# Kernel optimization log

Measured on AMD Instinct MI355X. Metric: run time of the kernel, lower is better.

## Reference

```python
import jax, jax.numpy as jnp
import numpy as np

K = 27        # 3^3 kernel offsets for kernel_size=3, dimension=3
M = 50000     # kernel-map pairs per offset
N = 100000    # active voxels
C = 64        # channels
EPS = 1e-5


def setup_inputs() -> dict:
    key = jax.random.key(0)
    ks = jax.random.split(key, 5)
    scale = 1.0 / np.sqrt(K * C)
    return {
        "features": jax.random.normal(ks[0], (N, C), jnp.float32),
        "W1": jax.random.normal(ks[1], (K, C, C), jnp.float32) * scale,
        "gamma1": jnp.ones((C,), jnp.float32),
        "beta1": jnp.zeros((C,), jnp.float32),
        "W2": jax.random.normal(ks[2], (K, C, C), jnp.float32) * scale,
        "gamma2": jnp.ones((C,), jnp.float32),
        "beta2": jnp.zeros((C,), jnp.float32),
        "in_maps": jax.random.randint(ks[3], (K, M), 0, N, dtype=jnp.int32),
        "out_maps": jax.random.randint(ks[4], (K, M), 0, N, dtype=jnp.int32),
        "n": N,
    }


def sparse_conv(f, W, in_maps, out_maps, n):
    # gather-GEMM-scatter, the MinkowskiConvolution compute pattern
    gathered = f[in_maps]                              # [K, M, Cin]
    msgs = jnp.einsum('kmc,kcd->kmd', gathered, W)     # [K, M, Cout]
    cout = W.shape[-1]
    out = jnp.zeros((n, cout), f.dtype)
    return out.at[out_maps.reshape(-1)].add(msgs.reshape(-1, cout))


def batch_norm(x, gamma, beta):
    # BatchNorm1d over the [N, C] sparse feature matrix (training-mode batch stats)
    mu = x.mean(axis=0)
    var = x.var(axis=0)
    return (x - mu) * jax.lax.rsqrt(var + EPS) * gamma + beta


def reference(features, W1, gamma1, beta1, W2, gamma2, beta2, in_maps, out_maps, n):
    out = sparse_conv(features, W1, in_maps, out_maps, n)
    out = jax.nn.relu(batch_norm(out, gamma1, beta1))
    out = sparse_conv(out, W2, in_maps, out_maps, n)
    out = batch_norm(out, gamma2, beta2)
    # stride=1 and in_channels==out_channels -> downsample is None
    return jax.nn.relu(out + features)
```

## Files before the change

### kernel.cpp

```cpp
#include <hip/hip_runtime.h>

typedef __attribute__((ext_vector_type(8))) short bf16x8;
typedef __attribute__((ext_vector_type(4))) float f32x4;

#define KK 27
#define MM 50000
#define NV 100000
#define CC 64
#define EPSV 1e-5f
#define PPB 400

__device__ inline void split2(float x, unsigned short& h, unsigned short& l) {
    const unsigned u  = __float_as_uint(x);
    const unsigned hb = u & 0xFFFF0000u;
    h = (unsigned short)(hb >> 16);
    const float r = x - __uint_as_float(hb);
    const unsigned v = __float_as_uint(r);
    l = (unsigned short)((v + 0x7FFFu + ((v >> 16) & 1u)) >> 16);
}

__device__ inline unsigned short rne_bf16(float x) {
    const unsigned u = __float_as_uint(x);
    return (unsigned short)((u + 0x7FFFu + ((u >> 16) & 1u)) >> 16);
}

__global__ __launch_bounds__(256)
void split_planes(const float* __restrict__ x, unsigned short* __restrict__ P) {
    const int i = blockIdx.x * 256 + threadIdx.x;
    const int r = i >> 5, c2 = (i & 31) * 2;
    const float2 v = *(const float2*)(x + (size_t)r * CC + c2);
    unsigned short h0, l0, h1, l1;
    split2(v.x, h0, l0);
    split2(v.y, h1, l1);
    *(unsigned int*)(P + (size_t)r * 128 + c2)      = (unsigned)h0 | ((unsigned)h1 << 16);
    *(unsigned int*)(P + (size_t)r * 128 + 64 + c2) = (unsigned)l0 | ((unsigned)l1 << 16);
}

__global__ __launch_bounds__(256)
void csr_hist(const int* __restrict__ outm, int* __restrict__ cnt) {
    const int e = blockIdx.x * 256 + threadIdx.x;
    if (e < KK * MM) atomicAdd(&cnt[outm[e]], 1);
}

__global__ __launch_bounds__(1024)
void scan1(const int* __restrict__ cnt, int* __restrict__ off, int* __restrict__ bsum) {
    __shared__ int tmp[1024];
    const int t = threadIdx.x;
    const int i = blockIdx.x * 1024 + t;
    const int v = (i < NV) ? cnt[i] : 0;
    tmp[t] = v;
    __syncthreads();
    for (int d = 1; d < 1024; d <<= 1) {
        const int add = (t >= d) ? tmp[t - d] : 0;
        __syncthreads();
        tmp[t] += add;
        __syncthreads();
    }
    if (i < NV) off[i] = tmp[t] - v;
    if (t == 1023) bsum[blockIdx.x] = tmp[1023];
}

__global__ __launch_bounds__(128)
void scan2(int* __restrict__ bsum, int nb) {
    __shared__ int tmp[128];
    const int t = threadIdx.x;
    const int v = (t < nb) ? bsum[t] : 0;
    tmp[t] = v;
    __syncthreads();
    for (int d = 1; d < 128; d <<= 1) {
        const int add = (t >= d) ? tmp[t - d] : 0;
        __syncthreads();
        tmp[t] += add;
        __syncthreads();
    }
    if (t < nb) bsum[t] = tmp[t] - v;
}

__global__ __launch_bounds__(256)
void scan3(int* __restrict__ off, const int* __restrict__ bsum) {
    const int i = blockIdx.x * 256 + threadIdx.x;
    if (i < NV) off[i] += bsum[i >> 10];
    if (i == 0) off[NV] = KK * MM;
}

__global__ __launch_bounds__(256)
void csr_fill(const int* __restrict__ outm, const int* __restrict__ off,
              int* __restrict__ cur, int* __restrict__ dst) {
    const int e = blockIdx.x * 256 + threadIdx.x;
    if (e >= KK * MM) return;
    const int row = outm[e];
    const int pos = atomicAdd(&cur[row], 1);
    dst[e] = off[row] + pos;
}

#define MF(a, b, c) c = __builtin_amdgcn_mfma_f32_16x16x32_bf16(a, b, c, 0, 0, 0)

struct AFrag { bf16x8 h0, h1, l0, l1; };

__device__ inline AFrag load_frag(const unsigned short* __restrict__ P,
                                  const int* __restrict__ inm, int base,
                                  int c16, int g) {
    const unsigned short* rp = P + (size_t)inm[base + c16] * 128 + g * 8;
    AFrag a;
    a.h0 = *(const bf16x8*)(rp);
    a.h1 = *(const bf16x8*)(rp + 32);
    a.l0 = *(const bf16x8*)(rp + 64);
    a.l1 = *(const bf16x8*)(rp + 96);
    return a;
}

__global__ __launch_bounds__(256)
void conv_gemm(const unsigned short* __restrict__ P, const float* __restrict__ W,
               const int* __restrict__ inm_all, const int* __restrict__ dst,
               unsigned short* __restrict__ msgs) {
    const int k   = blockIdx.y;
    const int L   = threadIdx.x & 63;
    const int wv  = threadIdx.x >> 6;
    const int g   = L >> 4;
    const int c16 = L & 15;

    __shared__ float lds[4352];

    {
        const float4* Wg  = (const float4*)(W + (size_t)k * CC * CC);
        float4*       Wl4 = (float4*)lds;
#pragma unroll
        for (int i = 0; i < 4; ++i)
            Wl4[threadIdx.x + 256 * i] = Wg[threadIdx.x + 256 * i];
    }
    __syncthreads();

    bf16x8 Wh[2][4], Wlo[2][4];
#pragma unroll
    for (int s = 0; s < 2; ++s)
#pragma unroll
        for (int t = 0; t < 4; ++t)
#pragma unroll
            for (int j = 0; j < 8; ++j) {
                const float w = lds[(g * 8 + j + 32 * s) * CC + 16 * t + c16];
                unsigned short h, lo;
                split2(w, h, lo);
                Wh[s][t][j]  = (short)h;
                Wlo[s][t][j] = (short)lo;
            }
    __syncthreads();

    float* ldsC = lds + wv * 1088;

    const int* inm = inm_all + (size_t)k * MM;
    const int pstart = blockIdx.x * PPB;
    const int pend   = min(MM, pstart + PPB);

    int b0 = pstart + wv * 16;
    if (b0 + 16 > pend) return;

    AFrag A0 = load_frag(P, inm, b0, c16, g);
    bool  v1 = (b0 + 80 <= pend);
    AFrag A1;
    if (v1) A1 = load_frag(P, inm, b0 + 64, c16, g);

    for (;;) {
        const bool v2 = (b0 + 144 <= pend);
        AFrag A2;
        if (v2) A2 = load_frag(P, inm, b0 + 128, c16, g);

        f32x4 acc0 = {0.f, 0.f, 0.f, 0.f}, acc1 = acc0, acc2 = acc0, acc3 = acc0;
        MF(A0.h0, Wh[0][0], acc0); MF(A0.h0, Wh[0][1], acc1); MF(A0.h0, Wh[0][2], acc2); MF(A0.h0, Wh[0][3], acc3);
        MF(A0.h1, Wh[1][0], acc0); MF(A0.h1, Wh[1][1], acc1); MF(A0.h1, Wh[1][2], acc2); MF(A0.h1, Wh[1][3], acc3);
        MF(A0.l0, Wh[0][0], acc0); MF(A0.l0, Wh[0][1], acc1); MF(A0.l0, Wh[0][2], acc2); MF(A0.l0, Wh[0][3], acc3);
        MF(A0.l1, Wh[1][0], acc0); MF(A0.l1, Wh[1][1], acc1); MF(A0.l1, Wh[1][2], acc2); MF(A0.l1, Wh[1][3], acc3);
        MF(A0.h0, Wlo[0][0], acc0); MF(A0.h0, Wlo[0][1], acc1); MF(A0.h0, Wlo[0][2], acc2); MF(A0.h0, Wlo[0][3], acc3);
        MF(A0.h1, Wlo[1][0], acc0); MF(A0.h1, Wlo[1][1], acc1); MF(A0.h1, Wlo[1][2], acc2); MF(A0.h1, Wlo[1][3], acc3);

#pragma unroll
        for (int j = 0; j < 4; ++j) {
            ldsC[(g * 4 + j) * 68 +      c16] = acc0[j];
            ldsC[(g * 4 + j) * 68 + 16 + c16] = acc1[j];
            ldsC[(g * 4 + j) * 68 + 32 + c16] = acc2[j];
            ldsC[(g * 4 + j) * 68 + 48 + c16] = acc3[j];
        }
        const int e0 = k * MM + b0;
#pragma unroll
        for (int r = 0; r < 16; ++r) {
            const int d = dst[e0 + r];
            __builtin_nontemporal_store(rne_bf16(ldsC[r * 68 + L]),
                                        &msgs[(size_t)d * CC + L]);
        }

        if (!v1) break;
        A0 = A1; A1 = A2; v1 = v2; b0 += 64;
    }
}

__global__ __launch_bounds__(256)
void csr_reduce(const unsigned short* __restrict__ msgs, const int* __restrict__ off,
                float* __restrict__ out) {
    const int L   = threadIdx.x & 63;
    const int wv  = threadIdx.x >> 6;
    const int n   = blockIdx.x * 4 + wv;
    if (n >= NV) return;
    const int q   = L & 15;
    const int sub = L >> 4;
    const int s = off[n], e = off[n + 1];
    float a0 = 0.f, a1 = 0.f, a2 = 0.f, a3 = 0.f;
    for (int i = s + sub; i < e; i += 4) {
        const uint2 v = *(const uint2*)(msgs + (size_t)i * CC + q * 4);
        a0 += __uint_as_float(v.x << 16);
        a1 += __uint_as_float(v.x & 0xFFFF0000u);
        a2 += __uint_as_float(v.y << 16);
        a3 += __uint_as_float(v.y & 0xFFFF0000u);
    }
    a0 += __shfl_xor(a0, 16); a1 += __shfl_xor(a1, 16);
    a2 += __shfl_xor(a2, 16); a3 += __shfl_xor(a3, 16);
    a0 += __shfl_xor(a0, 32); a1 += __shfl_xor(a1, 32);
    a2 += __shfl_xor(a2, 32); a3 += __shfl_xor(a3, 32);
    if (sub == 0) {
        const float4 r = {a0, a1, a2, a3};
        *(float4*)(out + (size_t)n * CC + q * 4) = r;
    }
}

__global__ __launch_bounds__(256)
void bn_stats(const float* __restrict__ x, float* __restrict__ stats) {
    const int c  = threadIdx.x & 63;
    const int rg = threadIdx.x >> 6;
    float s = 0.f, ss = 0.f;
    for (int r = blockIdx.x * 4 + rg; r < NV; r += gridDim.x * 4) {
        const float v = x[(size_t)r * CC + c];
        s += v;
        ss = fmaf(v, v, ss);
    }
    __shared__ float red[2][4][CC];
    red[0][rg][c] = s;
    red[1][rg][c] = ss;
    __syncthreads();
    if (threadIdx.x < CC) {
        const float ts  = red[0][0][c] + red[0][1][c] + red[0][2][c] + red[0][3][c];
        const float tss = red[1][0][c] + red[1][1][c] + red[1][2][c] + red[1][3][c];
        atomicAdd(&stats[c], ts);
        atomicAdd(&stats[CC + c], tss);
    }
}

__global__ __launch_bounds__(256)
void bn_relu_split(const float* __restrict__ x, const float* __restrict__ stats,
                   const float* __restrict__ gamma, const float* __restrict__ beta,
                   unsigned short* __restrict__ P) {
    const int i = blockIdx.x * 256 + threadIdx.x;
    const int r = i >> 5, c2 = (i & 31) * 2;
    float sc[2], sh[2];
#pragma unroll
    for (int j = 0; j < 2; ++j) {
        const int   c    = c2 + j;
        const float mu   = stats[c] * (1.f / NV);
        const float var  = fmaf(-mu, mu, stats[CC + c] * (1.f / NV));
        const float istd = rsqrtf(var + EPSV);
        sc[j] = gamma[c] * istd;
        sh[j] = fmaf(-mu, sc[j], beta[c]);
    }
    const float2 v = *(const float2*)(x + (size_t)r * CC + c2);
    const float y0 = fmaxf(fmaf(v.x, sc[0], sh[0]), 0.f);
    const float y1 = fmaxf(fmaf(v.y, sc[1], sh[1]), 0.f);
    unsigned short h0, l0, h1, l1;
    split2(y0, h0, l0);
    split2(y1, h1, l1);
    *(unsigned int*)(P + (size_t)r * 128 + c2)      = (unsigned)h0 | ((unsigned)h1 << 16);
    *(unsigned int*)(P + (size_t)r * 128 + 64 + c2) = (unsigned)l0 | ((unsigned)l1 << 16);
}

__global__ __launch_bounds__(256)
void bn_res_relu(float* __restrict__ x, const float* __restrict__ feat,
                 const float* __restrict__ stats,
                 const float* __restrict__ gamma, const float* __restrict__ beta) {
    const int tid   = blockIdx.x * blockDim.x + threadIdx.x;
    const int total = NV * CC / 4;
    const int cbase = (tid * 4) & (CC - 1);
    float scale[4], shift[4];
#pragma unroll
    for (int j = 0; j < 4; ++j) {
        const int   c    = cbase + j;
        const float mu   = stats[c] * (1.f / NV);
        const float var  = fmaf(-mu, mu, stats[CC + c] * (1.f / NV));
        const float istd = rsqrtf(var + EPSV);
        scale[j] = gamma[c] * istd;
        shift[j] = fmaf(-mu, scale[j], beta[c]);
    }
    float4*       x4 = (float4*)x;
    const float4* f4 = (const float4*)feat;
    for (int i = tid; i < total; i += gridDim.x * blockDim.x) {
        float4 v = x4[i];
        const float4 fr = f4[i];
        v.x = fmaxf(fmaf(v.x, scale[0], shift[0]) + fr.x, 0.f);
        v.y = fmaxf(fmaf(v.y, scale[1], shift[1]) + fr.y, 0.f);
        v.z = fmaxf(fmaf(v.z, scale[2], shift[2]) + fr.z, 0.f);
        v.w = fmaxf(fmaf(v.w, scale[3], shift[3]) + fr.w, 0.f);
        x4[i] = v;
    }
}

extern "C" void kernel_launch(void* const* d_in, const int* in_sizes, int n_in,
                              void* d_out, int out_size, void* d_ws, size_t ws_size,
                              hipStream_t stream) {
    const float* features = (const float*)d_in[0];
    const float* W1       = (const float*)d_in[1];
    const float* gamma1   = (const float*)d_in[2];
    const float* beta1    = (const float*)d_in[3];
    const float* W2       = (const float*)d_in[4];
    const float* gamma2   = (const float*)d_in[5];
    const float* beta2    = (const float*)d_in[6];
    const int*   in_maps  = (const int*)d_in[7];
    const int*   out_maps = (const int*)d_in[8];

    float* out = (float*)d_out;

    unsigned short* P     = (unsigned short*)d_ws;
    float*          stats = (float*)(P + (size_t)NV * 128);
    int*            cnt   = (int*)(stats + 256);
    int*            cur   = cnt + NV;
    int*            off   = cur + NV;
    int*            dst   = off + NV + 8;
    int*            bsum  = dst + KK * MM;
    unsigned short* msgs  = (unsigned short*)(bsum + 256);

    dim3 cgrid(MM / PPB, KK);

    hipMemsetAsync(stats, 0, (256 + 2 * NV) * sizeof(int), stream);

    split_planes<<<12500, 256, 0, stream>>>(features, P);

    csr_hist<<<(KK * MM + 255) / 256, 256, 0, stream>>>(out_maps, cnt);
    const int nb = (NV + 1023) / 1024;
    scan1<<<nb, 1024, 0, stream>>>(cnt, off, bsum);
    scan2<<<1, 128, 0, stream>>>(bsum, nb);
    scan3<<<(NV + 255) / 256, 256, 0, stream>>>(off, bsum);
    csr_fill<<<(KK * MM + 255) / 256, 256, 0, stream>>>(out_maps, off, cur, dst);

    conv_gemm<<<cgrid, 256, 0, stream>>>(P, W1, in_maps, dst, msgs);
    csr_reduce<<<NV / 4, 256, 0, stream>>>(msgs, off, out);
    bn_stats<<<800, 256, 0, stream>>>(out, stats);
    bn_relu_split<<<12500, 256, 0, stream>>>(out, stats, gamma1, beta1, P);

    conv_gemm<<<cgrid, 256, 0, stream>>>(P, W2, in_maps, dst, msgs);
    csr_reduce<<<NV / 4, 256, 0, stream>>>(msgs, off, out);
    bn_stats<<<800, 256, 0, stream>>>(out, stats + 128);
    bn_res_relu<<<1024, 256, 0, stream>>>(out, features, stats + 128, gamma2, beta2);
}
```

Measured before the change: 681.9 us.

## Fuse BN statistics into CSR reduction and simplify conv_gemm prefetch

New measurement: 599.6 us. 12.1% less time.

```diff
diff --git a/kernel.cpp b/kernel.cpp
--- a/kernel.cpp
+++ b/kernel.cpp
@@ -95,21 +95,7 @@
 
 #define MF(a, b, c) c = __builtin_amdgcn_mfma_f32_16x16x32_bf16(a, b, c, 0, 0, 0)
 
-struct AFrag { bf16x8 h0, h1, l0, l1; };
-
-__device__ inline AFrag load_frag(const unsigned short* __restrict__ P,
-                                  const int* __restrict__ inm, int base,
-                                  int c16, int g) {
-    const unsigned short* rp = P + (size_t)inm[base + c16] * 128 + g * 8;
-    AFrag a;
-    a.h0 = *(const bf16x8*)(rp);
-    a.h1 = *(const bf16x8*)(rp + 32);
-    a.l0 = *(const bf16x8*)(rp + 64);
-    a.l1 = *(const bf16x8*)(rp + 96);
-    return a;
-}
-
-__global__ __launch_bounds__(256)
+__global__ __launch_bounds__(256, 3)
 void conv_gemm(const unsigned short* __restrict__ P, const float* __restrict__ W,
                const int* __restrict__ inm_all, const int* __restrict__ dst,
                unsigned short* __restrict__ msgs) {
@@ -151,26 +137,34 @@
     const int pstart = blockIdx.x * PPB;
     const int pend   = min(MM, pstart + PPB);
 
-    int b0 = pstart + wv * 16;
-    if (b0 + 16 > pend) return;
-
-    AFrag A0 = load_frag(P, inm, b0, c16, g);
-    bool  v1 = (b0 + 80 <= pend);
-    AFrag A1;
-    if (v1) A1 = load_frag(P, inm, b0 + 64, c16, g);
-
-    for (;;) {
-        const bool v2 = (b0 + 144 <= pend);
-        AFrag A2;
-        if (v2) A2 = load_frag(P, inm, b0 + 128, c16, g);
+    int base = pstart + wv * 16;
+    if (base + 16 > pend) return;
+
+    const unsigned short* rp = P + (size_t)inm[base + c16] * 128;
+    bf16x8 ah0 = *(const bf16x8*)(rp +      g * 8);
+    bf16x8 ah1 = *(const bf16x8*)(rp + 32 + g * 8);
+    bf16x8 al0 = *(const bf16x8*)(rp + 64 + g * 8);
+    bf16x8 al1 = *(const bf16x8*)(rp + 96 + g * 8);
+
+    while (true) {
+        const int  nbase = base + 64;
+        const bool hasn  = (nbase + 16 <= pend);
+        bf16x8 nh0, nh1, nl0, nl1;
+        if (hasn) {
+            const unsigned short* np = P + (size_t)inm[nbase + c16] * 128;
+            nh0 = *(const bf16x8*)(np +      g * 8);
+            nh1 = *(const bf16x8*)(np + 32 + g * 8);
+            nl0 = *(const bf16x8*)(np + 64 + g * 8);
+            nl1 = *(const bf16x8*)(np + 96 + g * 8);
+        }
 
         f32x4 acc0 = {0.f, 0.f, 0.f, 0.f}, acc1 = acc0, acc2 = acc0, acc3 = acc0;
-        MF(A0.h0, Wh[0][0], acc0); MF(A0.h0, Wh[0][1], acc1); MF(A0.h0, Wh[0][2], acc2); MF(A0.h0, Wh[0][3], acc3);
-        MF(A0.h1, Wh[1][0], acc0); MF(A0.h1, Wh[1][1], acc1); MF(A0.h1, Wh[1][2], acc2); MF(A0.h1, Wh[1][3], acc3);
-        MF(A0.l0, Wh[0][0], acc0); MF(A0.l0, Wh[0][1], acc1); MF(A0.l0, Wh[0][2], acc2); MF(A0.l0, Wh[0][3], acc3);
-        MF(A0.l1, Wh[1][0], acc0); MF(A0.l1, Wh[1][1], acc1); MF(A0.l1, Wh[1][2], acc2); MF(A0.l1, Wh[1][3], acc3);
-        MF(A0.h0, Wlo[0][0], acc0); MF(A0.h0, Wlo[0][1], acc1); MF(A0.h0, Wlo[0][2], acc2); MF(A0.h0, Wlo[0][3], acc3);
-        MF(A0.h1, Wlo[1][0], acc0); MF(A0.h1, Wlo[1][1], acc1); MF(A0.h1, Wlo[1][2], acc2); MF(A0.h1, Wlo[1][3], acc3);
+        MF(ah0, Wh[0][0], acc0); MF(ah0, Wh[0][1], acc1); MF(ah0, Wh[0][2], acc2); MF(ah0, Wh[0][3], acc3);
+        MF(ah1, Wh[1][0], acc0); MF(ah1, Wh[1][1], acc1); MF(ah1, Wh[1][2], acc2); MF(ah1, Wh[1][3], acc3);
+        MF(al0, Wh[0][0], acc0); MF(al0, Wh[0][1], acc1); MF(al0, Wh[0][2], acc2); MF(al0, Wh[0][3], acc3);
+        MF(al1, Wh[1][0], acc0); MF(al1, Wh[1][1], acc1); MF(al1, Wh[1][2], acc2); MF(al1, Wh[1][3], acc3);
+        MF(ah0, Wlo[0][0], acc0); MF(ah0, Wlo[0][1], acc1); MF(ah0, Wlo[0][2], acc2); MF(ah0, Wlo[0][3], acc3);
+        MF(ah1, Wlo[1][0], acc0); MF(ah1, Wlo[1][1], acc1); MF(ah1, Wlo[1][2], acc2); MF(ah1, Wlo[1][3], acc3);
 
 #pragma unroll
         for (int j = 0; j < 4; ++j) {
@@ -179,62 +173,65 @@
             ldsC[(g * 4 + j) * 68 + 32 + c16] = acc2[j];
             ldsC[(g * 4 + j) * 68 + 48 + c16] = acc3[j];
         }
-        const int e0 = k * MM + b0;
+        const int e0 = k * MM + base;
 #pragma unroll
         for (int r = 0; r < 16; ++r) {
             const int d = dst[e0 + r];
-            __builtin_nontemporal_store(rne_bf16(ldsC[r * 68 + L]),
-                                        &msgs[(size_t)d * CC + L]);
-        }
-
-        if (!v1) break;
-        A0 = A1; A1 = A2; v1 = v2; b0 += 64;
-    }
-}
-
-__global__ __launch_bounds__(256)
-void csr_reduce(const unsigned short* __restrict__ msgs, const int* __restrict__ off,
-                float* __restrict__ out) {
+            msgs[(size_t)d * CC + L] = rne_bf16(ldsC[r * 68 + L]);
+        }
+
+        if (!hasn) break;
+        base = nbase;
+        ah0 = nh0; ah1 = nh1; al0 = nl0; al1 = nl1;
+    }
+}
+
+__global__ __launch_bounds__(256)
+void csr_reduce_stats(const unsigned short* __restrict__ msgs,
+                      const int* __restrict__ off,
+                      float* __restrict__ out, float* __restrict__ stats) {
     const int L   = threadIdx.x & 63;
     const int wv  = threadIdx.x >> 6;
-    const int n   = blockIdx.x * 4 + wv;
-    if (n >= NV) return;
     const int q   = L & 15;
     const int sub = L >> 4;
-    const int s = off[n], e = off[n + 1];
-    float a0 = 0.f, a1 = 0.f, a2 = 0.f, a3 = 0.f;
-    for (int i = s + sub; i < e; i += 4) {
-        const uint2 v = *(const uint2*)(msgs + (size_t)i * CC + q * 4);
-        a0 += __uint_as_float(v.x << 16);
-        a1 += __uint_as_float(v.x & 0xFFFF0000u);
-        a2 += __uint_as_float(v.y << 16);
-        a3 += __uint_as_float(v.y & 0xFFFF0000u);
-    }
-    a0 += __shfl_xor(a0, 16); a1 += __shfl_xor(a1, 16);
-    a2 += __shfl_xor(a2, 16); a3 += __shfl_xor(a3, 16);
-    a0 += __shfl_xor(a0, 32); a1 += __shfl_xor(a1, 32);
-    a2 += __shfl_xor(a2, 32); a3 += __shfl_xor(a3, 32);
+
+    float sum0 = 0.f, sum1 = 0.f, sum2 = 0.f, sum3 = 0.f;
+    float ssq0 = 0.f, ssq1 = 0.f, ssq2 = 0.f, ssq3 = 0.f;
+
+    for (int n = blockIdx.x * 4 + wv; n < NV; n += gridDim.x * 4) {
+        const int s = off[n], e = off[n + 1];
+        float a0 = 0.f, a1 = 0.f, a2 = 0.f, a3 = 0.f;
+        for (int i = s + sub; i < e; i += 4) {
+            const uint2 v = *(const uint2*)(msgs + (size_t)i * CC + q * 4);
+            a0 += __uint_as_float(v.x << 16);
+            a1 += __uint_as_float(v.x & 0xFFFF0000u);
+            a2 += __uint_as_float(v.y << 16);
+            a3 += __uint_as_float(v.y & 0xFFFF0000u);
+        }
+        a0 += __shfl_xor(a0, 16); a1 += __shfl_xor(a1, 16);
+        a2 += __shfl_xor(a2, 16); a3 += __shfl_xor(a3, 16);
+        a0 += __shfl_xor(a0, 32); a1 += __shfl_xor(a1, 32);
+        a2 += __shfl_xor(a2, 32); a3 += __shfl_xor(a3, 32);
+        if (sub == 0) {
+            const float4 r = {a0, a1, a2, a3};
+            *(float4*)(out + (size_t)n * CC + q * 4) = r;
+            sum0 += a0; ssq0 = fmaf(a0, a0, ssq0);
+            sum1 += a1; ssq1 = fmaf(a1, a1, ssq1);
+            sum2 += a2; ssq2 = fmaf(a2, a2, ssq2);
+            sum3 += a3; ssq3 = fmaf(a3, a3, ssq3);
+        }
+    }
+
+    __shared__ float red[2][4][CC];
     if (sub == 0) {
-        const float4 r = {a0, a1, a2, a3};
-        *(float4*)(out + (size_t)n * CC + q * 4) = r;
-    }
-}
-
-__global__ __launch_bounds__(256)
-void bn_stats(const float* __restrict__ x, float* __restrict__ stats) {
-    const int c  = threadIdx.x & 63;
-    const int rg = threadIdx.x >> 6;
-    float s = 0.f, ss = 0.f;
-    for (int r = blockIdx.x * 4 + rg; r < NV; r += gridDim.x * 4) {
-        const float v = x[(size_t)r * CC + c];
-        s += v;
-        ss = fmaf(v, v, ss);
-    }
-    __shared__ float red[2][4][CC];
-    red[0][rg][c] = s;
-    red[1][rg][c] = ss;
+        red[0][wv][q * 4 + 0] = sum0; red[1][wv][q * 4 + 0] = ssq0;
+        red[0][wv][q * 4 + 1] = sum1; red[1][wv][q * 4 + 1] = ssq1;
+        red[0][wv][q * 4 + 2] = sum2; red[1][wv][q * 4 + 2] = ssq2;
+        red[0][wv][q * 4 + 3] = sum3; red[1][wv][q * 4 + 3] = ssq3;
+    }
     __syncthreads();
     if (threadIdx.x < CC) {
+        const int c = threadIdx.x;
         const float ts  = red[0][0][c] + red[0][1][c] + red[0][2][c] + red[0][3][c];
         const float tss = red[1][0][c] + red[1][1][c] + red[1][2][c] + red[1][3][c];
         atomicAdd(&stats[c], ts);
@@ -336,12 +333,10 @@
     csr_fill<<<(KK * MM + 255) / 256, 256, 0, stream>>>(out_maps, off, cur, dst);
 
     conv_gemm<<<cgrid, 256, 0, stream>>>(P, W1, in_maps, dst, msgs);
-    csr_reduce<<<NV / 4, 256, 0, stream>>>(msgs, off, out);
-    bn_stats<<<800, 256, 0, stream>>>(out, stats);
+    csr_reduce_stats<<<2048, 256, 0, stream>>>(msgs, off, out, stats);
     bn_relu_split<<<12500, 256, 0, stream>>>(out, stats, gamma1, beta1, P);
 
     conv_gemm<<<cgrid, 256, 0, stream>>>(P, W2, in_maps, dst, msgs);
-    csr_reduce<<<NV / 4, 256, 0, stream>>>(msgs, off, out);
-    bn_stats<<<800, 256, 0, stream>>>(out, stats + 128);
+    csr_reduce_stats<<<2048, 256, 0, stream>>>(msgs, off, out, stats + 128);
     bn_res_relu<<<1024, 256, 0, stream>>>(out, features, stats + 128, gamma2, beta2);
 }
```
